# Optimization experiments

Measured on AMD Instinct MI355X. Metric: run time of the kernel, lower is better.

## Reference

```python
import jax, jax.numpy as jnp
import numpy as np

N_NODES = 100000
N_EDGES = 3200000
HID = 16


def _graph_conv(x, src, dst, w_rel, w_root, b_rel, num_nodes):
    # PyG GraphConv: out_i = lin_rel(sum_{j in N(i)} x_j) + lin_root(x_i)
    agg = jax.ops.segment_sum(x[src], dst, num_segments=num_nodes)  # [N, d_in]
    return agg @ w_rel + b_rel + x @ w_root


def setup_inputs() -> dict:
    key = jax.random.key(0)
    ks = jax.random.split(key, 8)
    x = jax.random.normal(ks[0], (N_NODES, 1), dtype=jnp.float32)
    edge_index = jax.random.randint(ks[1], (2, N_EDGES), 0, N_NODES, dtype=jnp.int64)
    s = 1.0 / np.sqrt(HID)
    return {
        "x": x,
        "edge_index": edge_index,
        "enc_w_rel": jax.random.uniform(ks[2], (1, HID), jnp.float32, -1.0, 1.0),
        "enc_w_root": jax.random.uniform(ks[3], (1, HID), jnp.float32, -1.0, 1.0),
        "enc_b": jnp.zeros((HID,), jnp.float32),
        "proc_w_rel": jax.random.uniform(ks[4], (HID, HID), jnp.float32, -s, s),
        "proc_w_root": jax.random.uniform(ks[5], (HID, HID), jnp.float32, -s, s),
        "proc_b": jnp.zeros((HID,), jnp.float32),
        "dec_w_rel": jax.random.uniform(ks[6], (HID, 1), jnp.float32, -s, s),
        "dec_w_root": jax.random.uniform(ks[7], (HID, 1), jnp.float32, -s, s),
        "dec_b": jnp.zeros((1,), jnp.float32),
    }


def reference(x, edge_index, enc_w_rel, enc_w_root, enc_b,
              proc_w_rel, proc_w_root, proc_b,
              dec_w_rel, dec_w_root, dec_b):
    num_nodes = x.shape[0]
    src, dst = edge_index[0], edge_index[1]
    z = _graph_conv(x, src, dst, enc_w_rel, enc_w_root, enc_b, num_nodes)
    z = jax.nn.relu(z)
    z = _graph_conv(z, src, dst, proc_w_rel, proc_w_root, proc_b, num_nodes)
    y = _graph_conv(z, src, dst, dec_w_rel, dec_w_root, dec_b, num_nodes)
    return jax.nn.relu(y)
```

## Files before the change

### kernel.cpp

```cpp
#include <hip/hip_runtime.h>
#include <hip/hip_bf16.h>

#define HID 16
#define SB_BITS 11
#define SBLK (1 << SB_BITS)
#define SUBS 128
#define NBMAX 64
#define GSTRIDE 16
#define PT_THREADS 256
#define PT_K 16
#define PT_EDGES (PT_THREADS * PT_K)
#define ROWP 65

__global__ void k_init(int* __restrict__ p, int n) {
    int i = blockIdx.x * blockDim.x + threadIdx.x;
    if (i < n) p[i] = 0;
}

__global__ void k_passA(const int* __restrict__ src, const int* __restrict__ dst,
                        unsigned* __restrict__ bucketsA, int* __restrict__ gcurA,
                        int E, int nb, int capA) {
    __shared__ int cnt[NBMAX];
    __shared__ int pos[NBMAX];
    __shared__ int gbase[NBMAX];
    __shared__ unsigned reorder[PT_EDGES];
    __shared__ unsigned char bbk[PT_EDGES];
    int tb = blockIdx.x * PT_EDGES;
    int nE = min(PT_EDGES, E - tb);
    if (threadIdx.x < nb) cnt[threadIdx.x] = 0;
    __syncthreads();
    int kk[PT_K]; int rk[PT_K]; unsigned pk[PT_K];
#pragma unroll
    for (int k = 0; k < PT_K; k++) {
        int e = tb + k * PT_THREADS + threadIdx.x;
        if (e < E) {
            int s = src[e], d = dst[e];
            int b = d >> SB_BITS;
            kk[k] = b;
            pk[k] = ((unsigned)(d & (SBLK - 1)) << 17) | (unsigned)s;
            rk[k] = atomicAdd(&cnt[b], 1);
        } else kk[k] = -1;
    }
    __syncthreads();
    if (threadIdx.x == 0) {
        int acc = 0;
        for (int b = 0; b < nb; b++) { pos[b] = acc; acc += cnt[b]; }
    }
    __syncthreads();
    if (threadIdx.x < nb && cnt[threadIdx.x] > 0)
        gbase[threadIdx.x] = atomicAdd(&gcurA[threadIdx.x * GSTRIDE], cnt[threadIdx.x]);
    __syncthreads();
#pragma unroll
    for (int k = 0; k < PT_K; k++) {
        if (kk[k] >= 0) {
            int idx = pos[kk[k]] + rk[k];
            reorder[idx] = pk[k];
            bbk[idx] = (unsigned char)kk[k];
        }
    }
    __syncthreads();
    for (int idx = threadIdx.x; idx < nE; idx += PT_THREADS) {
        int b = bbk[idx];
        int g = gbase[b] + (idx - pos[b]);
        if (g < capA) bucketsA[(size_t)b * capA + g] = reorder[idx];
    }
}

__global__ void k_passB(const unsigned* __restrict__ bucketsA, const int* __restrict__ gcurA,
                        unsigned* __restrict__ bucketsB, int* __restrict__ gcurB,
                        int capA, int capSub, int tilesB) {
    int j = blockIdx.x / tilesB;
    int tile = blockIdx.x - j * tilesB;
    int cnt_j = min(gcurA[j * GSTRIDE], capA);
    int tb = tile * PT_EDGES;
    if (tb >= cnt_j) return;
    int nE = min(PT_EDGES, cnt_j - tb);
    __shared__ int cnt[SUBS];
    __shared__ int pos[SUBS];
    __shared__ int gb[SUBS];
    __shared__ unsigned reorder[PT_EDGES];
    __shared__ unsigned char bbk[PT_EDGES];
    if (threadIdx.x < SUBS) cnt[threadIdx.x] = 0;
    __syncthreads();
    const unsigned* in = bucketsA + (size_t)j * capA + tb;
    int kk[PT_K]; int rk[PT_K]; unsigned pk[PT_K];
#pragma unroll
    for (int k = 0; k < PT_K; k++) {
        int e = k * PT_THREADS + threadIdx.x;
        if (e < nE) {
            unsigned p = in[e];
            int dloc = (int)(p >> 17);
            int s = dloc >> 4;
            kk[k] = s;
            pk[k] = ((p & 0x1FFFFu) << 4) | (unsigned)(dloc & 15);
            rk[k] = atomicAdd(&cnt[s], 1);
        } else kk[k] = -1;
    }
    __syncthreads();
    if (threadIdx.x == 0) {
        int acc = 0;
        for (int s = 0; s < SUBS; s++) { pos[s] = acc; acc += cnt[s]; }
    }
    __syncthreads();
    if (threadIdx.x < SUBS && cnt[threadIdx.x] > 0)
        gb[threadIdx.x] = atomicAdd(&gcurB[j * SUBS + threadIdx.x], cnt[threadIdx.x]);
    __syncthreads();
#pragma unroll
    for (int k = 0; k < PT_K; k++) {
        if (kk[k] >= 0) {
            int idx = pos[kk[k]] + rk[k];
            reorder[idx] = pk[k];
            bbk[idx] = (unsigned char)kk[k];
        }
    }
    __syncthreads();
    for (int idx = threadIdx.x; idx < nE; idx += PT_THREADS) {
        int s = bbk[idx];
        int g = gb[s] + (idx - pos[s]);
        if (g < capSub) bucketsB[(size_t)(j * SUBS + s) * capSub + g] = reorder[idx];
    }
}

__global__ void __launch_bounds__(256)
k_agg1enc(const unsigned* __restrict__ bk2, const int* __restrict__ gcurB,
          const float* __restrict__ x,
          const float* __restrict__ ewrel, const float* __restrict__ ewroot,
          const float* __restrict__ eb,
          const float* __restrict__ pwrel, const float* __restrict__ pwroot,
          const float* __restrict__ dwrel, const float* __restrict__ dwroot,
          float* __restrict__ SAB, float* __restrict__ G1, float* __restrict__ G2,
          int capSub, int N) {
    __shared__ float P[4 * 16 * ROWP];
    __shared__ float su1[HID], su2[HID], sv1[HID], sv2[HID];
    __shared__ float swr[HID], swo[HID], sbb[HID];
    int t = threadIdx.x;
    if (t < 64) {
        int k = t & 15, w = t >> 4;
        const float* M  = (w < 2) ? pwrel : pwroot;
        const float* vv = ((w & 1) == 0) ? dwrel : dwroot;
        float acc = 0.f;
        for (int h = 0; h < HID; h++) acc += M[k * HID + h] * vv[h];
        if (w == 0) su1[k] = acc;
        else if (w == 1) su2[k] = acc;
        else if (w == 2) sv1[k] = acc;
        else sv2[k] = acc;
    }
    if (t < HID) { swr[t] = ewrel[t]; swo[t] = ewroot[t]; sbb[t] = eb[t]; }
    int wv = t >> 6, lane = t & 63;
    int q = blockIdx.x * 4 + wv;
    float* p = P + wv * 16 * ROWP;
#pragma unroll
    for (int d = 0; d < 16; d++) p[d * ROWP + lane] = 0.f;
    __syncthreads();
    int cnt = min(gcurB[q], capSub);
    const unsigned* bk = bk2 + (size_t)q * capSub;
    int e = lane;
    for (; e + 64 < cnt; e += 128) {
        unsigned pk0 = bk[e], pk1 = bk[e + 64];
        float v0 = x[pk0 >> 4], v1 = x[pk1 >> 4];
        p[(int)(pk0 & 15) * ROWP + lane] += v0;
        p[(int)(pk1 & 15) * ROWP + lane] += v1;
    }
    if (e < cnt) { unsigned pk = bk[e]; p[(int)(pk & 15) * ROWP + lane] += x[pk >> 4]; }
    __builtin_amdgcn_wave_barrier();
    int d = lane & 15, c0 = (lane >> 4) * 16;
    float s = 0.f;
#pragma unroll
    for (int k = 0; k < 16; k++) s += p[d * ROWP + c0 + k];
    s += __shfl_xor(s, 16);
    s += __shfl_xor(s, 32);
    if (lane < 16) {
        int n = q * 16 + lane;
        if (n < N) {
            float a1 = s, xi = x[n];
            float sa = 0.f, sb = 0.f, g1 = 0.f, g2 = 0.f;
#pragma unroll
            for (int h = 0; h < HID; h++) {
                float z = fmaxf(fmaf(a1, swr[h], fmaf(xi, swo[h], sbb[h])), 0.f);
                sa = fmaf(z, su1[h], sa);
                sb = fmaf(z, su2[h], sb);
                g1 = fmaf(z, sv1[h], g1);
                g2 = fmaf(z, sv2[h], g2);
            }
            ((float2*)SAB)[n] = make_float2(sa, sb);
            G1[n] = g1; G2[n] = g2;
        }
    }
}

__global__ void __launch_bounds__(256)
k_agg2mid(const unsigned* __restrict__ bk2, const int* __restrict__ gcurB,
          const float* __restrict__ SAB,
          const float* __restrict__ G1, const float* __restrict__ G2,
          const float* __restrict__ pb, const float* __restrict__ dwrel,
          const float* __restrict__ dwroot, const float* __restrict__ db,
          float* __restrict__ BETA, float* __restrict__ R,
          int capSub, int N) {
    __shared__ float P[4 * 2 * 16 * ROWP];
    __shared__ float sc1, sc2, sbd;
    int t = threadIdx.x;
    if (t == 0) {
        float c1 = 0.f, c2 = 0.f;
        for (int h = 0; h < HID; h++) { c1 += pb[h] * dwrel[h]; c2 += pb[h] * dwroot[h]; }
        sc1 = c1; sc2 = c2; sbd = db[0];
    }
    int wv = t >> 6, lane = t & 63;
    int q = blockIdx.x * 4 + wv;
    float* pa = P + wv * 2 * 16 * ROWP;
    float* pbn = pa + 16 * ROWP;
#pragma unroll
    for (int d = 0; d < 16; d++) { pa[d * ROWP + lane] = 0.f; pbn[d * ROWP + lane] = 0.f; }
    __syncthreads();
    int cnt = min(gcurB[q], capSub);
    const unsigned* bk = bk2 + (size_t)q * capSub;
    const float2* v2 = (const float2*)SAB;
    int e = lane;
    for (; e + 64 < cnt; e += 128) {
        unsigned pk0 = bk[e], pk1 = bk[e + 64];
        float2 v0 = v2[pk0 >> 4], v1 = v2[pk1 >> 4];
        int a0 = (int)(pk0 & 15) * ROWP + lane;
        int a1 = (int)(pk1 & 15) * ROWP + lane;
        pa[a0] += v0.x; pbn[a0] += v0.y;
        pa[a1] += v1.x; pbn[a1] += v1.y;
    }
    if (e < cnt) {
        unsigned pk = bk[e];
        float2 v = v2[pk >> 4];
        int a = (int)(pk & 15) * ROWP + lane;
        pa[a] += v.x; pbn[a] += v.y;
    }
    __builtin_amdgcn_wave_barrier();
    int d = lane & 15, c0 = (lane >> 4) * 16;
    float sa = 0.f, sb = 0.f;
#pragma unroll
    for (int k = 0; k < 16; k++) {
        sa += pa[d * ROWP + c0 + k];
        sb += pbn[d * ROWP + c0 + k];
    }
    sa += __shfl_xor(sa, 16); sa += __shfl_xor(sa, 32);
    sb += __shfl_xor(sb, 16); sb += __shfl_xor(sb, 32);
    if (lane < 16) {
        int n = q * 16 + lane;
        if (n < N) {
            BETA[n] = sa + G1[n] + sc1;
            R[n]    = sb + G2[n] + sc2 + sbd;
        }
    }
}

__global__ void __launch_bounds__(256)
k_agg1f(const unsigned* __restrict__ bk2, const int* __restrict__ gcurB,
        const float* __restrict__ val, const float* __restrict__ R,
        float* __restrict__ out, int capSub, int N) {
    __shared__ float P[4 * 16 * ROWP];
    int wv = threadIdx.x >> 6, lane = threadIdx.x & 63;
    int q = blockIdx.x * 4 + wv;
    float* p = P + wv * 16 * ROWP;
#pragma unroll
    for (int d = 0; d < 16; d++) p[d * ROWP + lane] = 0.f;
    int cnt = min(gcurB[q], capSub);
    const unsigned* bk = bk2 + (size_t)q * capSub;
    int e = lane;
    for (; e + 64 < cnt; e += 128) {
        unsigned pk0 = bk[e], pk1 = bk[e + 64];
        float v0 = val[pk0 >> 4], v1 = val[pk1 >> 4];
        p[(int)(pk0 & 15) * ROWP + lane] += v0;
        p[(int)(pk1 & 15) * ROWP + lane] += v1;
    }
    if (e < cnt) { unsigned pk = bk[e]; p[(int)(pk & 15) * ROWP + lane] += val[pk >> 4]; }
    __builtin_amdgcn_wave_barrier();
    int d = lane & 15, c0 = (lane >> 4) * 16;
    float s = 0.f;
#pragma unroll
    for (int k = 0; k < 16; k++) s += p[d * ROWP + c0 + k];
    s += __shfl_xor(s, 16);
    s += __shfl_xor(s, 32);
    if (lane < 16) {
        int n = q * 16 + lane;
        if (n < N) out[n] = fmaxf(s + R[n], 0.f);
    }
}

extern "C" void kernel_launch(void* const* d_in, const int* in_sizes, int n_in,
                              void* d_out, int out_size, void* d_ws, size_t ws_size,
                              hipStream_t stream) {
    const float* x      = (const float*)d_in[0];
    const int*   ei     = (const int*)d_in[1];
    const float* ewrel  = (const float*)d_in[2];
    const float* ewroot = (const float*)d_in[3];
    const float* eb     = (const float*)d_in[4];
    const float* pwrel  = (const float*)d_in[5];
    const float* pwroot = (const float*)d_in[6];
    const float* pb     = (const float*)d_in[7];
    const float* dwrel  = (const float*)d_in[8];
    const float* dwroot = (const float*)d_in[9];
    const float* db     = (const float*)d_in[10];
    float* out = (float*)d_out;

    const int N = in_sizes[0];
    const int E = in_sizes[1] / 2;
    const int* src = ei;
    const int* dst = ei + E;

    const int nb = (N + SBLK - 1) >> SB_BITS;
    int capA = ((E / nb + 2048) + PT_EDGES - 1) & ~(PT_EDGES - 1);
    const int tilesB = capA / PT_EDGES;
    const int nq = nb * SUBS;
    int capSub = ((E / nq + 226) + 3) & ~3;

    size_t off = 0;
    int* gcurA = (int*)d_ws;                    off += NBMAX * GSTRIDE;
    int* gcurB = (int*)d_ws + off;              off += nq;
    const int zeroWords = (int)off;
    off = (off + 255) & ~(size_t)255;
    unsigned* bucketsA = (unsigned*)d_ws + off; off += (size_t)nb * capA;
    unsigned* bucketsB = (unsigned*)d_ws + off; off += (size_t)nq * capSub;
    float* SAB  = (float*)d_ws + off;           off += (size_t)2 * N;
    float* G1   = (float*)d_ws + off;           off += N;
    float* G2   = (float*)d_ws + off;           off += N;
    float* BETA = (float*)d_ws + off;           off += N;
    float* R    = (float*)d_ws + off;           off += N;

    const int ntilesA = (E + PT_EDGES - 1) / PT_EDGES;
    const int aggBlocks = nq / 4;

    hipLaunchKernelGGL(k_init, dim3((zeroWords + 255) / 256), dim3(256), 0, stream,
                       gcurA, zeroWords);
    hipLaunchKernelGGL(k_passA, dim3(ntilesA), dim3(PT_THREADS), 0, stream,
                       src, dst, bucketsA, gcurA, E, nb, capA);
    hipLaunchKernelGGL(k_passB, dim3(nb * tilesB), dim3(PT_THREADS), 0, stream,
                       bucketsA, gcurA, bucketsB, gcurB, capA, capSub, tilesB);

    hipLaunchKernelGGL(k_agg1enc, dim3(aggBlocks), dim3(256), 0, stream,
                       bucketsB, gcurB, x, ewrel, ewroot, eb, pwrel, pwroot,
                       dwrel, dwroot, SAB, G1, G2, capSub, N);
    hipLaunchKernelGGL(k_agg2mid, dim3(aggBlocks), dim3(256), 0, stream,
                       bucketsB, gcurB, SAB, G1, G2, pb, dwrel, dwroot, db,
                       BETA, R, capSub, N);
    hipLaunchKernelGGL(k_agg1f, dim3(aggBlocks), dim3(256), 0, stream,
                       bucketsB, gcurB, BETA, R, out, capSub, N);
}
```

Baseline: 182.7 us.

## Replace shared-memory atomics in bucket passes with ballot-based wave ranking

```diff
diff --git a/kernel.cpp b/kernel.cpp
--- a/kernel.cpp
+++ b/kernel.cpp
@@ -5,11 +5,10 @@
 #define SB_BITS 11
 #define SBLK (1 << SB_BITS)
 #define SUBS 128
-#define NBMAX 64
 #define GSTRIDE 16
-#define PT_THREADS 256
+#define PT 256
 #define PT_K 16
-#define PT_EDGES (PT_THREADS * PT_K)
+#define PT_EDGES (PT * PT_K)
 #define ROWP 65
 
 __global__ void k_init(int* __restrict__ p, int n) {
@@ -17,107 +16,153 @@
     if (i < n) p[i] = 0;
 }
 
-__global__ void k_passA(const int* __restrict__ src, const int* __restrict__ dst,
-                        unsigned* __restrict__ bucketsA, int* __restrict__ gcurA,
-                        int E, int nb, int capA) {
-    __shared__ int cnt[NBMAX];
-    __shared__ int pos[NBMAX];
-    __shared__ int gbase[NBMAX];
+template<int BITS>
+__device__ __forceinline__ int ballot_rank(int b, unsigned long long laneLT,
+                                           volatile int* wrow) {
+    unsigned long long m = ~0ull;
+#pragma unroll
+    for (int i = 0; i < BITS; i++) {
+        unsigned long long bi = __ballot((b >> i) & 1);
+        m &= ((b >> i) & 1) ? bi : ~bi;
+    }
+    int rank = (int)__popcll(m & laneLT);
+    int sz   = (int)__popcll(m);
+    if (rank == 0) wrow[b] += sz;
+    int after = wrow[b];
+    return after - sz + rank;
+}
+
+__global__ void __launch_bounds__(PT)
+k_passA(const int* __restrict__ src, const int* __restrict__ dst,
+        unsigned* __restrict__ bucketsA, int* __restrict__ gcurA,
+        int E, int nb, int capA) {
+    __shared__ int wcnt[4 * 64];
+    __shared__ int binTot[64];
+    __shared__ int pos[64];
+    __shared__ int gbase[64];
     __shared__ unsigned reorder[PT_EDGES];
     __shared__ unsigned char bbk[PT_EDGES];
+    int tid = threadIdx.x, w = tid >> 6, lane = tid & 63;
+    unsigned long long laneLT = (1ull << lane) - 1ull;
     int tb = blockIdx.x * PT_EDGES;
     int nE = min(PT_EDGES, E - tb);
-    if (threadIdx.x < nb) cnt[threadIdx.x] = 0;
-    __syncthreads();
-    int kk[PT_K]; int rk[PT_K]; unsigned pk[PT_K];
+    wcnt[tid] = 0;
+    __syncthreads();
+    volatile int* wrow = wcnt + w * 64;
+    unsigned pk[PT_K]; int kk[PT_K]; int rk[PT_K];
 #pragma unroll
     for (int k = 0; k < PT_K; k++) {
-        int e = tb + k * PT_THREADS + threadIdx.x;
+        int e = tb + k * PT + tid;
+        int b = 63;
+        unsigned p = 0;
         if (e < E) {
             int s = src[e], d = dst[e];
-            int b = d >> SB_BITS;
-            kk[k] = b;
-            pk[k] = ((unsigned)(d & (SBLK - 1)) << 17) | (unsigned)s;
-            rk[k] = atomicAdd(&cnt[b], 1);
-        } else kk[k] = -1;
-    }
-    __syncthreads();
-    if (threadIdx.x == 0) {
-        int acc = 0;
-        for (int b = 0; b < nb; b++) { pos[b] = acc; acc += cnt[b]; }
-    }
-    __syncthreads();
-    if (threadIdx.x < nb && cnt[threadIdx.x] > 0)
-        gbase[threadIdx.x] = atomicAdd(&gcurA[threadIdx.x * GSTRIDE], cnt[threadIdx.x]);
+            b = d >> SB_BITS;
+            p = ((unsigned)(d & (SBLK - 1)) << 17) | (unsigned)s;
+        }
+        kk[k] = b; pk[k] = p;
+        rk[k] = ballot_rank<6>(b, laneLT, wrow);
+    }
+    __syncthreads();
+    if (tid < 64) {
+        int c0 = wcnt[tid], c1 = wcnt[64 + tid], c2 = wcnt[128 + tid], c3 = wcnt[192 + tid];
+        wcnt[tid] = 0; wcnt[64 + tid] = c0; wcnt[128 + tid] = c0 + c1; wcnt[192 + tid] = c0 + c1 + c2;
+        binTot[tid] = c0 + c1 + c2 + c3;
+    }
+    __syncthreads();
+    if (tid < 64) {
+        int s = 0;
+        for (int j = 0; j < 64; j++) s += (j < tid) ? binTot[j] : 0;
+        pos[tid] = s;
+        gbase[tid] = (tid < nb && binTot[tid] > 0)
+                   ? atomicAdd(&gcurA[tid * GSTRIDE], binTot[tid]) : 0;
+    }
     __syncthreads();
 #pragma unroll
     for (int k = 0; k < PT_K; k++) {
-        if (kk[k] >= 0) {
-            int idx = pos[kk[k]] + rk[k];
+        int e = tb + k * PT + tid;
+        if (e < E) {
+            int b = kk[k];
+            int idx = pos[b] + wcnt[w * 64 + b] + rk[k];
             reorder[idx] = pk[k];
-            bbk[idx] = (unsigned char)kk[k];
-        }
-    }
-    __syncthreads();
-    for (int idx = threadIdx.x; idx < nE; idx += PT_THREADS) {
+            bbk[idx] = (unsigned char)b;
+        }
+    }
+    __syncthreads();
+    for (int idx = tid; idx < nE; idx += PT) {
         int b = bbk[idx];
         int g = gbase[b] + (idx - pos[b]);
         if (g < capA) bucketsA[(size_t)b * capA + g] = reorder[idx];
     }
 }
 
-__global__ void k_passB(const unsigned* __restrict__ bucketsA, const int* __restrict__ gcurA,
-                        unsigned* __restrict__ bucketsB, int* __restrict__ gcurB,
-                        int capA, int capSub, int tilesB) {
-    int j = blockIdx.x / tilesB;
-    int tile = blockIdx.x - j * tilesB;
-    int cnt_j = min(gcurA[j * GSTRIDE], capA);
-    int tb = tile * PT_EDGES;
-    if (tb >= cnt_j) return;
-    int nE = min(PT_EDGES, cnt_j - tb);
-    __shared__ int cnt[SUBS];
-    __shared__ int pos[SUBS];
-    __shared__ int gb[SUBS];
+__global__ void __launch_bounds__(PT)
+k_passB(const unsigned* __restrict__ bucketsA, const int* __restrict__ gcurA,
+        unsigned* __restrict__ bucketsB, int* __restrict__ gcurB,
+        int capA, int capSub, int tilesB) {
+    __shared__ int wcnt[4 * 256];
+    __shared__ int binTot[256];
+    __shared__ int pos[256];
+    __shared__ int gbase[256];
     __shared__ unsigned reorder[PT_EDGES];
     __shared__ unsigned char bbk[PT_EDGES];
-    if (threadIdx.x < SUBS) cnt[threadIdx.x] = 0;
-    __syncthreads();
-    const unsigned* in = bucketsA + (size_t)j * capA + tb;
-    int kk[PT_K]; int rk[PT_K]; unsigned pk[PT_K];
+    int row = blockIdx.x / tilesB;
+    int tile = blockIdx.x - row * tilesB;
+    int cnt_row = min(gcurA[row * GSTRIDE], capA);
+    int tb = tile * PT_EDGES;
+    if (tb >= cnt_row) return;
+    int nE = min(PT_EDGES, cnt_row - tb);
+    int tid = threadIdx.x, w = tid >> 6, lane = tid & 63;
+    unsigned long long laneLT = (1ull << lane) - 1ull;
+#pragma unroll
+    for (int i = 0; i < 4; i++) wcnt[i * 256 + tid] = 0;
+    __syncthreads();
+    volatile int* wrow = wcnt + w * 256;
+    const unsigned* in = bucketsA + (size_t)row * capA + tb;
+    unsigned pk[PT_K]; int kk[PT_K]; int rk[PT_K];
 #pragma unroll
     for (int k = 0; k < PT_K; k++) {
-        int e = k * PT_THREADS + threadIdx.x;
+        int e = k * PT + tid;
+        int b = 255;
+        unsigned p = 0;
         if (e < nE) {
-            unsigned p = in[e];
-            int dloc = (int)(p >> 17);
-            int s = dloc >> 4;
-            kk[k] = s;
-            pk[k] = ((p & 0x1FFFFu) << 4) | (unsigned)(dloc & 15);
-            rk[k] = atomicAdd(&cnt[s], 1);
-        } else kk[k] = -1;
-    }
-    __syncthreads();
-    if (threadIdx.x == 0) {
-        int acc = 0;
-        for (int s = 0; s < SUBS; s++) { pos[s] = acc; acc += cnt[s]; }
-    }
-    __syncthreads();
-    if (threadIdx.x < SUBS && cnt[threadIdx.x] > 0)
-        gb[threadIdx.x] = atomicAdd(&gcurB[j * SUBS + threadIdx.x], cnt[threadIdx.x]);
+            unsigned q = in[e];
+            b = (int)(q >> 21);
+            p = ((q & 0x1FFFFu) << 4) | ((q >> 17) & 15u);
+        }
+        kk[k] = b; pk[k] = p;
+        rk[k] = ballot_rank<8>(b, laneLT, wrow);
+    }
+    __syncthreads();
+    {
+        int c0 = wcnt[tid], c1 = wcnt[256 + tid], c2 = wcnt[512 + tid], c3 = wcnt[768 + tid];
+        wcnt[tid] = 0; wcnt[256 + tid] = c0; wcnt[512 + tid] = c0 + c1; wcnt[768 + tid] = c0 + c1 + c2;
+        binTot[tid] = c0 + c1 + c2 + c3;
+    }
+    __syncthreads();
+    if (tid < 128) {
+        int s = 0;
+        for (int j = 0; j < 128; j++) s += (j < tid) ? binTot[j] : 0;
+        pos[tid] = s;
+        gbase[tid] = (binTot[tid] > 0)
+                   ? atomicAdd(&gcurB[row * SUBS + tid], binTot[tid]) : 0;
+    }
     __syncthreads();
 #pragma unroll
     for (int k = 0; k < PT_K; k++) {
-        if (kk[k] >= 0) {
-            int idx = pos[kk[k]] + rk[k];
+        int e = k * PT + tid;
+        if (e < nE) {
+            int b = kk[k];
+            int idx = pos[b] + wcnt[w * 256 + b] + rk[k];
             reorder[idx] = pk[k];
-            bbk[idx] = (unsigned char)kk[k];
-        }
-    }
-    __syncthreads();
-    for (int idx = threadIdx.x; idx < nE; idx += PT_THREADS) {
-        int s = bbk[idx];
-        int g = gb[s] + (idx - pos[s]);
-        if (g < capSub) bucketsB[(size_t)(j * SUBS + s) * capSub + g] = reorder[idx];
+            bbk[idx] = (unsigned char)b;
+        }
+    }
+    __syncthreads();
+    for (int idx = tid; idx < nE; idx += PT) {
+        int b = bbk[idx];
+        int g = gbase[b] + (idx - pos[b]);
+        if (g < capSub) bucketsB[(size_t)(row * SUBS + b) * capSub + g] = reorder[idx];
     }
 }
 
@@ -155,6 +200,14 @@
     int cnt = min(gcurB[q], capSub);
     const unsigned* bk = bk2 + (size_t)q * capSub;
     int e = lane;
+    for (; e + 192 < cnt; e += 256) {
+        unsigned pk0 = bk[e], pk1 = bk[e + 64], pk2 = bk[e + 128], pk3 = bk[e + 192];
+        float v0 = x[pk0 >> 4], v1 = x[pk1 >> 4], v2 = x[pk2 >> 4], v3 = x[pk3 >> 4];
+        p[(int)(pk0 & 15) * ROWP + lane] += v0;
+        p[(int)(pk1 & 15) * ROWP + lane] += v1;
+        p[(int)(pk2 & 15) * ROWP + lane] += v2;
+        p[(int)(pk3 & 15) * ROWP + lane] += v3;
+    }
     for (; e + 64 < cnt; e += 128) {
         unsigned pk0 = bk[e], pk1 = bk[e + 64];
         float v0 = x[pk0 >> 4], v1 = x[pk1 >> 4];
@@ -215,6 +268,18 @@
     const unsigned* bk = bk2 + (size_t)q * capSub;
     const float2* v2 = (const float2*)SAB;
     int e = lane;
+    for (; e + 192 < cnt; e += 256) {
+        unsigned pk0 = bk[e], pk1 = bk[e + 64], pk2 = bk[e + 128], pk3 = bk[e + 192];
+        float2 v0 = v2[pk0 >> 4], v1 = v2[pk1 >> 4], w2 = v2[pk2 >> 4], w3 = v2[pk3 >> 4];
+        int a0 = (int)(pk0 & 15) * ROWP + lane;
+        int a1 = (int)(pk1 & 15) * ROWP + lane;
+        int a2 = (int)(pk2 & 15) * ROWP + lane;
+        int a3 = (int)(pk3 & 15) * ROWP + lane;
+        pa[a0] += v0.x; pbn[a0] += v0.y;
+        pa[a1] += v1.x; pbn[a1] += v1.y;
+        pa[a2] += w2.x; pbn[a2] += w2.y;
+        pa[a3] += w3.x; pbn[a3] += w3.y;
+    }
     for (; e + 64 < cnt; e += 128) {
         unsigned pk0 = bk[e], pk1 = bk[e + 64];
         float2 v0 = v2[pk0 >> 4], v1 = v2[pk1 >> 4];
@@ -261,6 +326,14 @@
     int cnt = min(gcurB[q], capSub);
     const unsigned* bk = bk2 + (size_t)q * capSub;
     int e = lane;
+    for (; e + 192 < cnt; e += 256) {
+        unsigned pk0 = bk[e], pk1 = bk[e + 64], pk2 = bk[e + 128], pk3 = bk[e + 192];
+        float v0 = val[pk0 >> 4], v1 = val[pk1 >> 4], v2 = val[pk2 >> 4], v3 = val[pk3 >> 4];
+        p[(int)(pk0 & 15) * ROWP + lane] += v0;
+        p[(int)(pk1 & 15) * ROWP + lane] += v1;
+        p[(int)(pk2 & 15) * ROWP + lane] += v2;
+        p[(int)(pk3 & 15) * ROWP + lane] += v3;
+    }
     for (; e + 64 < cnt; e += 128) {
         unsigned pk0 = bk[e], pk1 = bk[e + 64];
         float v0 = val[pk0 >> 4], v1 = val[pk1 >> 4];
@@ -309,7 +382,7 @@
     int capSub = ((E / nq + 226) + 3) & ~3;
 
     size_t off = 0;
-    int* gcurA = (int*)d_ws;                    off += NBMAX * GSTRIDE;
+    int* gcurA = (int*)d_ws;                    off += (size_t)64 * GSTRIDE;
     int* gcurB = (int*)d_ws + off;              off += nq;
     const int zeroWords = (int)off;
     off = (off + 255) & ~(size_t)255;
@@ -326,9 +399,9 @@
 
     hipLaunchKernelGGL(k_init, dim3((zeroWords + 255) / 256), dim3(256), 0, stream,
                        gcurA, zeroWords);
-    hipLaunchKernelGGL(k_passA, dim3(ntilesA), dim3(PT_THREADS), 0, stream,
+    hipLaunchKernelGGL(k_passA, dim3(ntilesA), dim3(PT), 0, stream,
                        src, dst, bucketsA, gcurA, E, nb, capA);
-    hipLaunchKernelGGL(k_passB, dim3(nb * tilesB), dim3(PT_THREADS), 0, stream,
+    hipLaunchKernelGGL(k_passB, dim3(nb * tilesB), dim3(PT), 0, stream,
                        bucketsA, gcurA, bucketsB, gcurB, capA, capSub, tilesB);
 
     hipLaunchKernelGGL(k_agg1enc, dim3(aggBlocks), dim3(256), 0, stream,
```

Result: slower. 210.0 us (+15.0%).
